# Optimization experiments

Hardware: AMD Instinct MI355X
Metric: run time of the kernel (lower is better)

The kernel has to match this reference:

```python
import jax, jax.numpy as jnp
import numpy as np

FEAT = 512
COND = 768
N_HEADS = 8
D_HEAD = 64
D_ATTN = N_HEADS * D_HEAD  # 512


def setup_inputs() -> dict:
    key = jax.random.key(0)
    ks = jax.random.split(key, 8)
    B, N, M = 16, 4096, 77
    x = jax.random.normal(ks[0], (B, N, FEAT), dtype=jnp.float32)
    cond = jax.random.normal(ks[1], (B, M, COND), dtype=jnp.float32)
    s_f = 1.0 / np.sqrt(FEAT)
    s_c = 1.0 / np.sqrt(COND)
    s_a = 1.0 / np.sqrt(D_ATTN)
    Wq = jax.random.normal(ks[2], (FEAT, D_ATTN), dtype=jnp.float32) * s_f
    Wk = jax.random.normal(ks[3], (COND, D_ATTN), dtype=jnp.float32) * s_c
    Wv = jax.random.normal(ks[4], (COND, D_ATTN), dtype=jnp.float32) * s_c
    Wo = jax.random.normal(ks[5], (D_ATTN, FEAT), dtype=jnp.float32) * s_a
    bo = jax.random.normal(ks[6], (FEAT,), dtype=jnp.float32) * 0.01
    return {"x": x, "cond": cond, "Wq": Wq, "Wk": Wk, "Wv": Wv, "Wo": Wo, "bo": bo}


def reference(x, cond, Wq, Wk, Wv, Wo, bo):
    B, N, _ = x.shape
    M = cond.shape[1]
    scale = D_HEAD ** (-0.5)
    # projections (no bias, as in nn.Linear(..., bias=False))
    q = (x @ Wq).reshape(B, N, N_HEADS, D_HEAD)
    k = (cond @ Wk).reshape(B, M, N_HEADS, D_HEAD)
    v = (cond @ Wv).reshape(B, M, N_HEADS, D_HEAD)
    attn = jnp.einsum('bihd,bjhd->bhij', q, k) * scale  # [B,H,N,M]
    attn = jax.nn.softmax(attn, axis=-1)  # split-half inplace softmax == plain softmax
    out = jnp.einsum('bhij,bjhd->bihd', attn, v).reshape(B, N, D_ATTN)
    return out @ Wo + bo
```

## Files before the change

### kernel.cpp

```cpp
#include <hip/hip_runtime.h>

typedef __attribute__((ext_vector_type(8))) _Float16 f16x8;
typedef __attribute__((ext_vector_type(4))) float f32x4;

#define B_SZ   16
#define N_SEQ  4096
#define M_CTX  77
#define M_PAD  96
#define NH     8

__device__ __forceinline__ _Float16 f2h(float x) { return (_Float16)x; }

__device__ __forceinline__ void gload16(const void* g, void* l) {
    __builtin_amdgcn_global_load_lds(
        (const __attribute__((address_space(1))) unsigned int*)g,
        (__attribute__((address_space(3))) unsigned int*)l, 16, 0, 0);
}

#define BAR()    asm volatile("s_barrier" ::: "memory")
#define WAITV8() asm volatile("s_waitcnt vmcnt(8)" ::: "memory")

template<int C>
__device__ __forceinline__ float dppf(float x) {
    union { float f; int i; } u, v;
    u.f = x;
    v.i = __builtin_amdgcn_mov_dpp(u.i, C, 0xF, 0xF, true);
    return v.f;
}
__device__ __forceinline__ float rmax16(float x) {
    x = fmaxf(x, dppf<0xB1>(x));
    x = fmaxf(x, dppf<0x4E>(x));
    x = fmaxf(x, dppf<0x141>(x));
    x = fmaxf(x, dppf<0x140>(x));
    return x;
}
__device__ __forceinline__ float rsum16(float x) {
    x += dppf<0xB1>(x);
    x += dppf<0x4E>(x);
    x += dppf<0x141>(x);
    x += dppf<0x140>(x);
    return x;
}

__global__ __launch_bounds__(256)
void convert(const float4* __restrict__ x, f16x8* __restrict__ xh, int n8)
{
    int idx = blockIdx.x * 256 + threadIdx.x;
    int stride = gridDim.x * 256;
    for (int i = idx; i < n8; i += stride) {
        float4 a = x[2 * i];
        float4 b = x[2 * i + 1];
        f16x8 o;
        o[0] = f2h(a.x); o[1] = f2h(a.y); o[2] = f2h(a.z); o[3] = f2h(a.w);
        o[4] = f2h(b.x); o[5] = f2h(b.y); o[6] = f2h(b.z); o[7] = f2h(b.w);
        xh[i] = o;
    }
}

__global__ __launch_bounds__(256)
void prep(const float* __restrict__ Wq, const float* __restrict__ Wk,
          const float* __restrict__ Wv, const float* __restrict__ Wo,
          _Float16* __restrict__ WqT, _Float16* __restrict__ WkT,
          _Float16* __restrict__ WvT, _Float16* __restrict__ WoT)
{
    __shared__ float t[32][33];
    const float* W; _Float16* WT; int K; float scale = 1.0f;
    switch (blockIdx.z) {
        case 0:  W = Wq; WT = WqT; K = 512; scale = 0.125f; break;
        case 1:  W = Wk; WT = WkT; K = 768; break;
        case 2:  W = Wv; WT = WvT; K = 768; break;
        default: W = Wo; WT = WoT; K = 512; break;
    }
    const int ky = blockIdx.y;
    if (ky * 32 >= K) return;
    const int nx = blockIdx.x;
    const int tr = threadIdx.x >> 5, tc = threadIdx.x & 31;
#pragma unroll
    for (int i = 0; i < 4; ++i) {
        int kr = tr + i * 8;
        t[kr][tc] = W[(size_t)(ky * 32 + kr) * 512 + nx * 32 + tc];
    }
    __syncthreads();
#pragma unroll
    for (int i = 0; i < 4; ++i) {
        int nr = tr + i * 8;
        WT[(size_t)(nx * 32 + nr) * K + ky * 32 + tc] = f2h(t[tc][nr] * scale);
    }
}

__global__ __launch_bounds__(256)
void kv_proj(const float* __restrict__ cond, const _Float16* __restrict__ WkT,
             const _Float16* __restrict__ WvT, _Float16* __restrict__ Kswz,
             _Float16* __restrict__ Vswz)
{
    const int tid = threadIdx.x;
    const int l = tid & 63, w = tid >> 6;
    const int lrow = l & 15, lk = l >> 4;
    const int h = blockIdx.x, b = blockIdx.y, which = blockIdx.z;
    const _Float16* WT = which ? WvT : WkT;
    const float* cb = cond + (size_t)b * M_CTX * 768;

    f32x4 acc[5];
#pragma unroll
    for (int i = 0; i < 5; ++i)
#pragma unroll
        for (int e = 0; e < 4; ++e) acc[i][e] = 0.f;

    const int n = h * 64 + w * 16 + lrow;
    for (int kk = 0; kk < 24; ++kk) {
        f16x8 bfrag = *(const f16x8*)(WT + (size_t)n * 768 + kk * 32 + lk * 8);
#pragma unroll
        for (int rt = 0; rt < 5; ++rt) {
            int m = rt * 16 + lrow;
            f16x8 afrag;
#pragma unroll
            for (int j = 0; j < 8; ++j) afrag[j] = (_Float16)0.f;
            if (m < M_CTX) {
                const float* a = cb + (size_t)m * 768 + kk * 32 + lk * 8;
                float4 f0 = *(const float4*)a;
                float4 f1 = *(const float4*)(a + 4);
                afrag[0] = f2h(f0.x); afrag[1] = f2h(f0.y);
                afrag[2] = f2h(f0.z); afrag[3] = f2h(f0.w);
                afrag[4] = f2h(f1.x); afrag[5] = f2h(f1.y);
                afrag[6] = f2h(f1.z); afrag[7] = f2h(f1.w);
            }
            acc[rt] = __builtin_amdgcn_mfma_f32_16x16x32_f16(afrag, bfrag, acc[rt], 0, 0, 0);
        }
    }

    const int bh = b * NH + h;
    const int d = w * 16 + lrow;
    const int dhi = d >> 3, dlo = d & 7;
    if (which == 0) {
        _Float16* Kb = Kswz + (size_t)bh * (M_PAD * 64);
#pragma unroll
        for (int rt = 0; rt < 5; ++rt)
#pragma unroll
            for (int r = 0; r < 4; ++r) {
                int m = rt * 16 + lk * 4 + r;
                Kb[m * 64 + ((dhi ^ (m & 7)) * 8) + dlo] = f2h(acc[rt][r]);
            }
#pragma unroll
        for (int r = 0; r < 4; ++r) {
            int m = 80 + lk * 4 + r;
            Kb[m * 64 + ((dhi ^ (m & 7)) * 8) + dlo] = (_Float16)0.f;
        }
    } else {
        _Float16* Vb = Vswz + (size_t)bh * (64 * 128);
#pragma unroll
        for (int rt = 0; rt < 5; ++rt)
#pragma unroll
            for (int r = 0; r < 4; ++r) {
                int m = rt * 16 + lk * 4 + r;
                Vb[d * 128 + (((m >> 3) ^ dlo) * 8) + (m & 7)] = f2h(acc[rt][r]);
            }
#pragma unroll
        for (int r = 0; r < 4; ++r) {
            int m = 80 + lk * 4 + r;
            Vb[d * 128 + (((m >> 3) ^ dlo) * 8) + (m & 7)] = (_Float16)0.f;
        }
    }
}

template<int EMODE>
__global__ __launch_bounds__(512)
void gemm_pipe(const _Float16* __restrict__ A, const _Float16* __restrict__ BT,
               void* __restrict__ Cv, const float* __restrict__ bias)
{
    __shared__ _Float16 L[4 * 16384];

    const int bid = blockIdx.x;
    const int wg = (bid & 7) * 64 + (bid >> 3);
    const size_t row0 = (size_t)(wg >> 1) * 256;
    const int col0 = (wg & 1) * 256;

    const int tid = threadIdx.x;
    const int l = tid & 63, w = tid >> 6;
    const int wy = w >> 2, wx = w & 3;
    const int lrow = l & 15, lk = l >> 4;

    const int srow  = l >> 2;
    const int sslot = ((l & 3) - srow) & 3;
    const _Float16* a_src = A  + (row0 + (size_t)(w * 32 + srow)) * 512 + sslot * 8;
    const _Float16* b_src = BT + ((size_t)col0 + w * 32 + srow) * 512 + sslot * 8;

    auto stage = [&](int t) {
        _Float16* dA = &L[(t & 3) * 16384 + w * 1024];
        _Float16* dB = dA + 8192;
        const _Float16* sA = a_src + t * 32;
        const _Float16* sB = b_src + t * 32;
        gload16(sA,            dA);
        gload16(sA + 16 * 512, dA + 512);
        gload16(sB,            dB);
        gload16(sB + 16 * 512, dB + 512);
    };

    f32x4 acc[8][4];
#pragma unroll
    for (int i = 0; i < 8; ++i)
#pragma unroll
        for (int j = 0; j < 4; ++j)
#pragma unroll
            for (int e = 0; e < 4; ++e) acc[i][j][e] = 0.f;

    stage(0); stage(1); stage(2);

    const int rdoff = ((lk + lrow) & 3) * 8;
    const int aoff = (wy * 128 + lrow) * 32 + rdoff;
    const int boff = 8192 + (wx * 64 + lrow) * 32 + rdoff;

    for (int kt = 0; kt < 16; ++kt) {
        WAITV8();
        BAR();
        if (kt + 3 < 16) stage(kt + 3);

        const _Float16* Lb = &L[(kt & 3) * 16384];
        f16x8 af[8], bf[4];
#pragma unroll
        for (int mt = 0; mt < 8; ++mt)
            af[mt] = *(const f16x8*)(Lb + aoff + mt * 512);
#pragma unroll
        for (int nt = 0; nt < 4; ++nt)
            bf[nt] = *(const f16x8*)(Lb + boff + nt * 512);

        __builtin_amdgcn_s_setprio(1);
#pragma unroll
        for (int mt = 0; mt < 8; ++mt)
#pragma unroll
            for (int nt = 0; nt < 4; ++nt)
                acc[mt][nt] = __builtin_amdgcn_mfma_f32_16x16x32_f16(af[mt], bf[nt], acc[mt][nt], 0, 0, 0);
        __builtin_amdgcn_s_setprio(0);
    }

#pragma unroll
    for (int mt = 0; mt < 8; ++mt)
#pragma unroll
        for (int nt = 0; nt < 4; ++nt)
#pragma unroll
            for (int r = 0; r < 4; ++r) {
                size_t row = row0 + wy * 128 + mt * 16 + lk * 4 + r;
                int col = col0 + wx * 64 + nt * 16 + lrow;
                float v = acc[mt][nt][r];
                if (EMODE == 0) {
                    ((_Float16*)Cv)[row * 512 + col] = f2h(v);
                } else {
                    ((float*)Cv)[row * 512 + col] = v + bias[col];
                }
            }
}

__global__ __launch_bounds__(256)
void attn(const _Float16* __restrict__ Q, const _Float16* __restrict__ Kswz,
          const _Float16* __restrict__ Vswz, _Float16* __restrict__ AO)
{
    __shared__ _Float16 Ks[M_PAD * 64];
    __shared__ _Float16 Vs[64 * 128];
    __shared__ _Float16 Pl[4][16][104];

    const int tid = threadIdx.x;
    const int l = tid & 63, w = tid >> 6;
    const int lrow = l & 15, lk = l >> 4;
    const int chunk = blockIdx.x, h = blockIdx.y, b = blockIdx.z;
    const int bh = b * NH + h;

    {
        const _Float16* Kg = Kswz + (size_t)bh * (M_PAD * 64);
        const _Float16* Vg = Vswz + (size_t)bh * (64 * 128);
#pragma unroll
        for (int i = 0; i < 3; ++i) {
            int c = w * 3 + i;
            gload16(Kg + c * 512 + l * 8, Ks + c * 512);
        }
#pragma unroll
        for (int i = 0; i < 4; ++i) {
            int c = w * 4 + i;
            gload16(Vg + c * 512 + l * 8, Vs + c * 512);
        }
    }

    const size_t row0 = (size_t)b * N_SEQ + chunk * 256 + w * 64;
    f16x8 af[4][2];
    {
        const _Float16* Qb = Q + (row0 + lrow) * 512 + h * 64 + lk * 8;
#pragma unroll
        for (int mt = 0; mt < 4; ++mt)
#pragma unroll
            for (int kk = 0; kk < 2; ++kk)
                af[mt][kk] = *(const f16x8*)(Qb + (size_t)mt * 16 * 512 + kk * 32);
    }

    for (int idx = l; idx < 256; idx += 64)
        Pl[w][idx >> 4][80 + (idx & 15)] = (_Float16)0.f;

    __syncthreads();

    const bool m4ok = (lrow < 13);
    const int kswz = lrow & 7;

#pragma unroll
    for (int mt = 0; mt < 4; ++mt) {
        f32x4 s[5];
#pragma unroll
        for (int i = 0; i < 5; ++i)
#pragma unroll
            for (int e = 0; e < 4; ++e) s[i][e] = 0.f;
#pragma unroll
        for (int kk = 0; kk < 2; ++kk)
#pragma unroll
            for (int ct = 0; ct < 5; ++ct) {
                f16x8 kf = *(const f16x8*)&Ks[(ct * 16 + lrow) * 64 + (((kk * 4 + lk) ^ kswz) * 8)];
                s[ct] = __builtin_amdgcn_mfma_f32_16x16x32_f16(af[mt][kk], kf, s[ct], 0, 0, 0);
            }

        float rinv[4];
#pragma unroll
        for (int r = 0; r < 4; ++r) {
            float v0 = s[0][r], v1 = s[1][r], v2 = s[2][r], v3 = s[3][r], v4 = s[4][r];
            float mx = fmaxf(fmaxf(v0, v1), fmaxf(v2, v3));
            mx = fmaxf(mx, m4ok ? v4 : -1e30f);
            mx = rmax16(mx);
            float e0 = __expf(v0 - mx), e1 = __expf(v1 - mx);
            float e2 = __expf(v2 - mx), e3 = __expf(v3 - mx);
            float e4 = m4ok ? __expf(v4 - mx) : 0.f;
            float sum = ((e0 + e1) + (e2 + e3)) + e4;
            sum = rsum16(sum);
            rinv[r] = 1.0f / sum;
            int prow = lk * 4 + r;
            Pl[w][prow][lrow]      = f2h(e0);
            Pl[w][prow][16 + lrow] = f2h(e1);
            Pl[w][prow][32 + lrow] = f2h(e2);
            Pl[w][prow][48 + lrow] = f2h(e3);
            Pl[w][prow][64 + lrow] = f2h(e4);
        }

        f32x4 o[4];
#pragma unroll
        for (int i = 0; i < 4; ++i)
#pragma unroll
            for (int e2 = 0; e2 < 4; ++e2) o[i][e2] = 0.f;
#pragma unroll
        for (int kk = 0; kk < 3; ++kk) {
            f16x8 pa = *(const f16x8*)&Pl[w][lrow][kk * 32 + lk * 8];
#pragma unroll
            for (int ctd = 0; ctd < 4; ++ctd) {
                f16x8 vf = *(const f16x8*)&Vs[(ctd * 16 + lrow) * 128 + (((kk * 4 + lk) ^ kswz) * 8)];
                o[ctd] = __builtin_amdgcn_mfma_f32_16x16x32_f16(pa, vf, o[ctd], 0, 0, 0);
            }
        }

        const size_t rw = row0 + mt * 16 + lk * 4;
#pragma unroll
        for (int ctd = 0; ctd < 4; ++ctd)
#pragma unroll
            for (int r = 0; r < 4; ++r)
                AO[(rw + r) * 512 + h * 64 + ctd * 16 + lrow] = f2h(o[ctd][r] * rinv[r]);
    }
}

extern "C" void kernel_launch(void* const* d_in, const int* in_sizes, int n_in,
                              void* d_out, int out_size, void* d_ws, size_t ws_size,
                              hipStream_t stream)
{
    (void)in_sizes; (void)n_in; (void)out_size; (void)ws_size;
    const float* x    = (const float*)d_in[0];
    const float* cond = (const float*)d_in[1];
    const float* Wq   = (const float*)d_in[2];
    const float* Wk   = (const float*)d_in[3];
    const float* Wv   = (const float*)d_in[4];
    const float* Wo   = (const float*)d_in[5];
    const float* bo   = (const float*)d_in[6];

    char* ws = (char*)d_ws;
    _Float16* WqT  = (_Float16*)(ws);
    _Float16* WoT  = (_Float16*)(ws + 524288);
    _Float16* Kswz = (_Float16*)(ws + 1048576);
    _Float16* Vswz = (_Float16*)(ws + 2621440);
    _Float16* xh   = (_Float16*)(ws + 4718592);
    _Float16* WkT  = (_Float16*)(ws + 4718592);
    _Float16* WvT  = (_Float16*)(ws + 4718592 + 786432);
    _Float16* AO   = xh;
    _Float16* Qf   = (_Float16*)d_out;

    prep<<<dim3(16, 24, 4), 256, 0, stream>>>(Wq, Wk, Wv, Wo, WqT, WkT, WvT, WoT);
    kv_proj<<<dim3(8, 16, 2), 256, 0, stream>>>(cond, WkT, WvT, Kswz, Vswz);
    convert<<<dim3(2048), 256, 0, stream>>>((const float4*)x, (f16x8*)xh, 16 * 4096 * 512 / 8);
    gemm_pipe<0><<<dim3(512), 512, 0, stream>>>(xh, WqT, Qf, nullptr);
    attn<<<dim3(16, 8, 16), 256, 0, stream>>>(Qf, Kswz, Vswz, AO);
    gemm_pipe<1><<<dim3(512), 512, 0, stream>>>(AO, WoT, d_out, bo);
}
```

Measured before the change: 227.1 us.

## Pre-tile GEMM operands into K-tile-contiguous blocks and store Q head-major

The converted x, the attention output, and the Wq/Wo weights are now written in a tiled layout where each 128-row by 32-K tile is contiguous, so each GEMM stage loads whole contiguous 1 KB blocks instead of strided rows with XOR swizzle offsets. Q is written head-major so the attention kernel reads each head's 64-wide slice contiguously. The GEMM main loop is also peeled to drop the per-iteration bound check and to drain with exact vmcnt waits. The cost is scattered 64-byte stores in the producers and LDS reads without the old swizzle, which may raise bank conflicts.

```diff
diff --git a/kernel.cpp b/kernel.cpp
--- a/kernel.cpp
+++ b/kernel.cpp
@@ -8,6 +8,7 @@
 #define M_CTX  77
 #define M_PAD  96
 #define NH     8
+#define NROWS  65536
 
 __device__ __forceinline__ _Float16 f2h(float x) { return (_Float16)x; }
 
@@ -19,6 +20,8 @@
 
 #define BAR()    asm volatile("s_barrier" ::: "memory")
 #define WAITV8() asm volatile("s_waitcnt vmcnt(8)" ::: "memory")
+#define WAITV4() asm volatile("s_waitcnt vmcnt(4)" ::: "memory")
+#define WAITV0() asm volatile("s_waitcnt vmcnt(0)" ::: "memory")
 
 template<int C>
 __device__ __forceinline__ float dppf(float x) {
@@ -43,37 +46,33 @@
 }
 
 __global__ __launch_bounds__(256)
-void convert(const float4* __restrict__ x, f16x8* __restrict__ xh, int n8)
+void convert_t(const float* __restrict__ x, f16x8* __restrict__ xhT, int n8)
 {
     int idx = blockIdx.x * 256 + threadIdx.x;
     int stride = gridDim.x * 256;
-    for (int i = idx; i < n8; i += stride) {
-        float4 a = x[2 * i];
-        float4 b = x[2 * i + 1];
+    for (int g = idx; g < n8; g += stride) {
+        int c8 = g & 3;
+        int r  = (g >> 2) & 127;
+        int kt = (g >> 9) & 15;
+        int rb = g >> 13;
+        const float* a = x + ((size_t)(rb * 128 + r) * 512 + kt * 32 + c8 * 8);
+        float4 f0 = *(const float4*)a;
+        float4 f1 = *(const float4*)(a + 4);
         f16x8 o;
-        o[0] = f2h(a.x); o[1] = f2h(a.y); o[2] = f2h(a.z); o[3] = f2h(a.w);
-        o[4] = f2h(b.x); o[5] = f2h(b.y); o[6] = f2h(b.z); o[7] = f2h(b.w);
-        xh[i] = o;
+        o[0] = f2h(f0.x); o[1] = f2h(f0.y); o[2] = f2h(f0.z); o[3] = f2h(f0.w);
+        o[4] = f2h(f1.x); o[5] = f2h(f1.y); o[6] = f2h(f1.z); o[7] = f2h(f1.w);
+        xhT[g] = o;
     }
 }
 
 __global__ __launch_bounds__(256)
-void prep(const float* __restrict__ Wq, const float* __restrict__ Wk,
-          const float* __restrict__ Wv, const float* __restrict__ Wo,
-          _Float16* __restrict__ WqT, _Float16* __restrict__ WkT,
-          _Float16* __restrict__ WvT, _Float16* __restrict__ WoT)
+void prep(const float* __restrict__ Wk, const float* __restrict__ Wv,
+          _Float16* __restrict__ WkT, _Float16* __restrict__ WvT)
 {
     __shared__ float t[32][33];
-    const float* W; _Float16* WT; int K; float scale = 1.0f;
-    switch (blockIdx.z) {
-        case 0:  W = Wq; WT = WqT; K = 512; scale = 0.125f; break;
-        case 1:  W = Wk; WT = WkT; K = 768; break;
-        case 2:  W = Wv; WT = WvT; K = 768; break;
-        default: W = Wo; WT = WoT; K = 512; break;
-    }
-    const int ky = blockIdx.y;
-    if (ky * 32 >= K) return;
-    const int nx = blockIdx.x;
+    const float* W = blockIdx.z ? Wv : Wk;
+    _Float16* WT   = blockIdx.z ? WvT : WkT;
+    const int ky = blockIdx.y, nx = blockIdx.x;
     const int tr = threadIdx.x >> 5, tc = threadIdx.x & 31;
 #pragma unroll
     for (int i = 0; i < 4; ++i) {
@@ -84,7 +83,33 @@
 #pragma unroll
     for (int i = 0; i < 4; ++i) {
         int nr = tr + i * 8;
-        WT[(size_t)(nx * 32 + nr) * K + ky * 32 + tc] = f2h(t[tc][nr] * scale);
+        WT[(size_t)(nx * 32 + nr) * 768 + ky * 32 + tc] = f2h(t[tc][nr]);
+    }
+}
+
+__global__ __launch_bounds__(256)
+void prep_bt(const float* __restrict__ Wq, const float* __restrict__ Wo,
+             _Float16* __restrict__ WqTt, _Float16* __restrict__ WoTt)
+{
+    __shared__ float t[32][33];
+    const float* W = blockIdx.z ? Wo : Wq;
+    _Float16* WT   = blockIdx.z ? WoTt : WqTt;
+    const float scale = blockIdx.z ? 1.0f : 0.125f;
+    const int kt = blockIdx.y, nx = blockIdx.x;
+    const int tr = threadIdx.x >> 5, tc = threadIdx.x & 31;
+#pragma unroll
+    for (int i = 0; i < 4; ++i) {
+        int kr = tr + i * 8;
+        t[kr][tc] = W[(size_t)(kt * 32 + kr) * 512 + nx * 32 + tc];
+    }
+    __syncthreads();
+    const int cb = nx >> 3;
+    const int nbase = (nx & 7) * 32;
+#pragma unroll
+    for (int i = 0; i < 4; ++i) {
+        int nr = tr + i * 8;
+        WT[((size_t)(cb * 16 + kt) * 256 + nbase + nr) * 32 + tc] =
+            f2h(t[tc][nr] * scale);
     }
 }
 
@@ -164,35 +189,36 @@
 
 template<int EMODE>
 __global__ __launch_bounds__(512)
-void gemm_pipe(const _Float16* __restrict__ A, const _Float16* __restrict__ BT,
+void gemm_pipe(const _Float16* __restrict__ At, const _Float16* __restrict__ Bt,
                void* __restrict__ Cv, const float* __restrict__ bias)
 {
     __shared__ _Float16 L[4 * 16384];
 
     const int bid = blockIdx.x;
     const int wg = (bid & 7) * 64 + (bid >> 3);
-    const size_t row0 = (size_t)(wg >> 1) * 256;
-    const int col0 = (wg & 1) * 256;
+    const int rb0 = (wg >> 1) * 2;
+    const size_t row0 = (size_t)rb0 * 128;
+    const int cb = wg & 1;
 
     const int tid = threadIdx.x;
     const int l = tid & 63, w = tid >> 6;
     const int wy = w >> 2, wx = w & 3;
     const int lrow = l & 15, lk = l >> 4;
 
-    const int srow  = l >> 2;
-    const int sslot = ((l & 3) - srow) & 3;
-    const _Float16* a_src = A  + (row0 + (size_t)(w * 32 + srow)) * 512 + sslot * 8;
-    const _Float16* b_src = BT + ((size_t)col0 + w * 32 + srow) * 512 + sslot * 8;
+    const int achunk = w >> 2;
+    const int aoffw  = (w & 3) * 1024;
+    const _Float16* a_base = At + ((size_t)(rb0 + achunk) * 16) * 4096 + aoffw + l * 8;
+    const _Float16* b_base = Bt + ((size_t)cb * 16) * 8192 + w * 1024 + l * 8;
 
     auto stage = [&](int t) {
         _Float16* dA = &L[(t & 3) * 16384 + w * 1024];
         _Float16* dB = dA + 8192;
-        const _Float16* sA = a_src + t * 32;
-        const _Float16* sB = b_src + t * 32;
-        gload16(sA,            dA);
-        gload16(sA + 16 * 512, dA + 512);
-        gload16(sB,            dB);
-        gload16(sB + 16 * 512, dB + 512);
+        const _Float16* sA = a_base + t * 4096;
+        const _Float16* sB = b_base + t * 8192;
+        gload16(sA,       dA);
+        gload16(sA + 512, dA + 512);
+        gload16(sB,       dB);
+        gload16(sB + 512, dB + 512);
     };
 
     f32x4 acc[8][4];
@@ -205,24 +231,18 @@
 
     stage(0); stage(1); stage(2);
 
-    const int rdoff = ((lk + lrow) & 3) * 8;
-    const int aoff = (wy * 128 + lrow) * 32 + rdoff;
-    const int boff = 8192 + (wx * 64 + lrow) * 32 + rdoff;
-
-    for (int kt = 0; kt < 16; ++kt) {
-        WAITV8();
-        BAR();
-        if (kt + 3 < 16) stage(kt + 3);
-
+    const int ar = (wy * 128 + lrow) * 32 + lk * 8;
+    const int br = 8192 + (wx * 64 + lrow) * 32 + lk * 8;
+
+    auto compute = [&](int kt) {
         const _Float16* Lb = &L[(kt & 3) * 16384];
         f16x8 af[8], bf[4];
 #pragma unroll
         for (int mt = 0; mt < 8; ++mt)
-            af[mt] = *(const f16x8*)(Lb + aoff + mt * 512);
+            af[mt] = *(const f16x8*)(Lb + ar + mt * 512);
 #pragma unroll
         for (int nt = 0; nt < 4; ++nt)
-            bf[nt] = *(const f16x8*)(Lb + boff + nt * 512);
-
+            bf[nt] = *(const f16x8*)(Lb + br + nt * 512);
         __builtin_amdgcn_s_setprio(1);
 #pragma unroll
         for (int mt = 0; mt < 8; ++mt)
@@ -230,7 +250,16 @@
             for (int nt = 0; nt < 4; ++nt)
                 acc[mt][nt] = __builtin_amdgcn_mfma_f32_16x16x32_f16(af[mt], bf[nt], acc[mt][nt], 0, 0, 0);
         __builtin_amdgcn_s_setprio(0);
-    }
+    };
+
+    for (int kt = 0; kt < 14; ++kt) {
+        WAITV8();
+        BAR();
+        stage(kt + 3);
+        compute(kt);
+    }
+    WAITV4(); BAR(); compute(14);
+    WAITV0(); BAR(); compute(15);
 
 #pragma unroll
     for (int mt = 0; mt < 8; ++mt)
@@ -239,10 +268,11 @@
 #pragma unroll
             for (int r = 0; r < 4; ++r) {
                 size_t row = row0 + wy * 128 + mt * 16 + lk * 4 + r;
-                int col = col0 + wx * 64 + nt * 16 + lrow;
+                int col = cb * 256 + wx * 64 + nt * 16 + lrow;
                 float v = acc[mt][nt][r];
                 if (EMODE == 0) {
-                    ((_Float16*)Cv)[row * 512 + col] = f2h(v);
+                    int h = col >> 6;
+                    ((_Float16*)Cv)[((size_t)h * NROWS + row) * 64 + (col & 63)] = f2h(v);
                 } else {
                     ((float*)Cv)[row * 512 + col] = v + bias[col];
                 }
@@ -250,8 +280,8 @@
 }
 
 __global__ __launch_bounds__(256)
-void attn(const _Float16* __restrict__ Q, const _Float16* __restrict__ Kswz,
-          const _Float16* __restrict__ Vswz, _Float16* __restrict__ AO)
+void attn(const _Float16* __restrict__ Qhm, const _Float16* __restrict__ Kswz,
+          const _Float16* __restrict__ Vswz, _Float16* __restrict__ AOt)
 {
     __shared__ _Float16 Ks[M_PAD * 64];
     __shared__ _Float16 Vs[64 * 128];
@@ -281,12 +311,12 @@
     const size_t row0 = (size_t)b * N_SEQ + chunk * 256 + w * 64;
     f16x8 af[4][2];
     {
-        const _Float16* Qb = Q + (row0 + lrow) * 512 + h * 64 + lk * 8;
+        const _Float16* Qb = Qhm + ((size_t)h * NROWS + row0 + lrow) * 64 + lk * 8;
 #pragma unroll
         for (int mt = 0; mt < 4; ++mt)
 #pragma unroll
             for (int kk = 0; kk < 2; ++kk)
-                af[mt][kk] = *(const f16x8*)(Qb + (size_t)mt * 16 * 512 + kk * 32);
+                af[mt][kk] = *(const f16x8*)(Qb + (size_t)mt * 16 * 64 + kk * 32);
     }
 
     for (int idx = l; idx < 256; idx += 64)
@@ -350,10 +380,16 @@
 
         const size_t rw = row0 + mt * 16 + lk * 4;
 #pragma unroll
-        for (int ctd = 0; ctd < 4; ++ctd)
-#pragma unroll
-            for (int r = 0; r < 4; ++r)
-                AO[(rw + r) * 512 + h * 64 + ctd * 16 + lrow] = f2h(o[ctd][r] * rinv[r]);
+        for (int ctd = 0; ctd < 4; ++ctd) {
+            const int ktc = (h << 1) | (ctd >> 1);
+            const int c = ((ctd & 1) << 4) | lrow;
+#pragma unroll
+            for (int r = 0; r < 4; ++r) {
+                size_t g = rw + r;
+                AOt[(((g >> 7) * 16 + ktc) * 128 + (g & 127)) * 32 + c] =
+                    f2h(o[ctd][r] * rinv[r]);
+            }
+        }
     }
 }
 
@@ -371,20 +407,21 @@
     const float* bo   = (const float*)d_in[6];
 
     char* ws = (char*)d_ws;
-    _Float16* WqT  = (_Float16*)(ws);
-    _Float16* WoT  = (_Float16*)(ws + 524288);
+    _Float16* WqTt = (_Float16*)(ws);
+    _Float16* WoTt = (_Float16*)(ws + 524288);
     _Float16* Kswz = (_Float16*)(ws + 1048576);
     _Float16* Vswz = (_Float16*)(ws + 2621440);
-    _Float16* xh   = (_Float16*)(ws + 4718592);
+    _Float16* xhT  = (_Float16*)(ws + 4718592);
     _Float16* WkT  = (_Float16*)(ws + 4718592);
     _Float16* WvT  = (_Float16*)(ws + 4718592 + 786432);
-    _Float16* AO   = xh;
-    _Float16* Qf   = (_Float16*)d_out;
-
-    prep<<<dim3(16, 24, 4), 256, 0, stream>>>(Wq, Wk, Wv, Wo, WqT, WkT, WvT, WoT);
+    _Float16* AOt  = xhT;
+    _Float16* Qhm  = (_Float16*)d_out;
+
+    prep<<<dim3(16, 24, 2), 256, 0, stream>>>(Wk, Wv, WkT, WvT);
+    prep_bt<<<dim3(16, 16, 2), 256, 0, stream>>>(Wq, Wo, WqTt, WoTt);
     kv_proj<<<dim3(8, 16, 2), 256, 0, stream>>>(cond, WkT, WvT, Kswz, Vswz);
-    convert<<<dim3(2048), 256, 0, stream>>>((const float4*)x, (f16x8*)xh, 16 * 4096 * 512 / 8);
-    gemm_pipe<0><<<dim3(512), 512, 0, stream>>>(xh, WqT, Qf, nullptr);
-    attn<<<dim3(16, 8, 16), 256, 0, stream>>>(Qf, Kswz, Vswz, AO);
-    gemm_pipe<1><<<dim3(512), 512, 0, stream>>>(AO, WoT, d_out, bo);
-}
+    convert_t<<<dim3(2048), 256, 0, stream>>>(x, (f16x8*)xhT, NROWS * 512 / 8);
+    gemm_pipe<0><<<dim3(512), 512, 0, stream>>>(xhT, WqTt, Qhm, nullptr);
+    attn<<<dim3(16, 8, 16), 256, 0, stream>>>(Qhm, Kswz, Vswz, AOt);
+    gemm_pipe<1><<<dim3(512), 512, 0, stream>>>(AOt, WoTt, d_out, bo);
+}
```

After: 233.5 us. 2.8% more time.
